# Kernel optimization log

Hardware: AMD Instinct MI355X
Metric: run time of the kernel (lower is better)

## Reference

```python
import jax, jax.numpy as jnp
import numpy as np

B, N, F, H, MH = 8, 1024, 768, 12, 3072
DH = F // H
EPS = 1e-5

def _ln(x, g, b):
    mu = jnp.mean(x, axis=-1, keepdims=True)
    var = jnp.mean(jnp.square(x - mu), axis=-1, keepdims=True)
    return (x - mu) * jax.lax.rsqrt(var + EPS) * g + b

def setup_inputs() -> dict:
    key = jax.random.key(0)
    ks = jax.random.split(key, 16)
    s = 1.0 / np.sqrt(F)
    sm = 1.0 / np.sqrt(MH)
    return {
        "x": jax.random.normal(ks[0], (B, N, F), dtype=jnp.float32),
        "Wq": jax.random.uniform(ks[1], (F, F), jnp.float32, -s, s),
        "bq": jax.random.uniform(ks[2], (F,), jnp.float32, -s, s),
        "Wk": jax.random.uniform(ks[3], (F, F), jnp.float32, -s, s),
        "bk": jax.random.uniform(ks[4], (F,), jnp.float32, -s, s),
        "Wv": jax.random.uniform(ks[5], (F, F), jnp.float32, -s, s),
        "bv": jax.random.uniform(ks[6], (F,), jnp.float32, -s, s),
        "Wo": jax.random.uniform(ks[7], (F, F), jnp.float32, -s, s),
        "bo": jax.random.uniform(ks[8], (F,), jnp.float32, -s, s),
        "ln1_g": jnp.ones((F,), jnp.float32),
        "ln1_b": jnp.zeros((F,), jnp.float32),
        "ln2_g": jnp.ones((F,), jnp.float32),
        "ln2_b": jnp.zeros((F,), jnp.float32),
        "W1": jax.random.uniform(ks[9], (F, MH), jnp.float32, -s, s),
        "b1": jax.random.uniform(ks[10], (MH,), jnp.float32, -s, s),
        "W2": jax.random.uniform(ks[11], (MH, F), jnp.float32, -sm, sm),
        "b2": jax.random.uniform(ks[12], (F,), jnp.float32, -sm, sm),
    }

def reference(x, Wq, bq, Wk, bk, Wv, bv, Wo, bo, ln1_g, ln1_b, ln2_g, ln2_b, W1, b1, W2, b2):
    xn = _ln(x, ln1_g, ln1_b)
    # low-rank (here full-rank, rank=-1) QKV projections, split into heads -> [b,h,n,dh]
    q = (xn @ Wq + bq).reshape(B, N, H, DH).transpose(0, 2, 1, 3)
    k = (xn @ Wk + bk).reshape(B, N, H, DH).transpose(0, 2, 1, 3)
    v = (xn @ Wv + bv).reshape(B, N, H, DH).transpose(0, 2, 1, 3)
    # note: original scales by sqrt(feats), NOT sqrt(d_head)
    score = jax.nn.softmax(jnp.einsum('bhif,bhjf->bhij', q, k) / jnp.sqrt(jnp.float32(F)), axis=-1)
    attn = jnp.einsum('bhij,bhjf->bhif', score, v)
    attn = attn.transpose(0, 2, 1, 3).reshape(B, N, F)
    out = (attn @ Wo + bo) + x  # dropout p=0.0
    h = _ln(out, ln2_g, ln2_b)
    h = jax.nn.gelu(h @ W1 + b1, approximate=False)
    h = jax.nn.gelu(h @ W2 + b2, approximate=False)  # second GELU per source
    return h + out
```

## Files before the change

### kernel.cpp

```cpp
#include <hip/hip_runtime.h>
#include <math.h>

#define B_ 8
#define N_ 1024
#define F_ 768
#define H_ 12
#define DH_ 64
#define MH_ 3072
#define MROWS (B_ * N_)

typedef unsigned short u16;
typedef unsigned int u32;
typedef __bf16 bf16x8 __attribute__((ext_vector_type(8)));
typedef float f32x4 __attribute__((ext_vector_type(4)));

__device__ inline f32x4 mfma16(bf16x8 a, bf16x8 b, f32x4 c) {
  return __builtin_amdgcn_mfma_f32_16x16x32_bf16(a, b, c, 0, 0, 0);
}

__device__ inline u16 f2bu(float f) {
  u32 b = __builtin_bit_cast(u32, f);
  b += 0x7fffu + ((b >> 16) & 1u);
  return (u16)(b >> 16);
}
__device__ inline float bu2f(u16 u) {
  u32 x = ((u32)u) << 16;
  return __builtin_bit_cast(float, x);
}
__device__ inline float gelu_exact(float x) {
  return 0.5f * x * (1.0f + erff(x * 0.70710678118654752f));
}

#define AS1 __attribute__((address_space(1)))
#define AS3 __attribute__((address_space(3)))
__device__ inline void glds16(const void* g, void* l) {
  __builtin_amdgcn_global_load_lds((const AS1 void*)g, (AS3 void*)l, 16, 0, 0);
}

__global__ __launch_bounds__(256) void prep_weights(
    const float* __restrict__ Wq, const float* __restrict__ Wk,
    const float* __restrict__ Wv, const float* __restrict__ Wo,
    const float* __restrict__ W1, const float* __restrict__ W2,
    u16* __restrict__ Wqkvt, u16* __restrict__ Wot,
    u16* __restrict__ W1t, u16* __restrict__ W2t) {
  __shared__ float tile[64][65];
  int z = blockIdx.z;
  const float* in; u16* out; int R, C;
  if (z == 0)      { in = Wq; out = Wqkvt;                       R = 768;  C = 768; }
  else if (z == 1) { in = Wk; out = Wqkvt + 768 * 768;           R = 768;  C = 768; }
  else if (z == 2) { in = Wv; out = Wqkvt + 2 * 768 * 768;       R = 768;  C = 768; }
  else if (z == 3) { in = Wo; out = Wot;                         R = 768;  C = 768; }
  else if (z == 4) { in = W1; out = W1t;                         R = 768;  C = 3072; }
  else             { in = W2; out = W2t;                         R = 3072; C = 768; }
  int r0 = blockIdx.y << 6, c0 = blockIdx.x << 6;
  if (r0 >= R || c0 >= C) return;
  int t = threadIdx.x;
#pragma unroll
  for (int i = 0; i < 16; ++i) {
    int idx = t + (i << 8);
    int r = idx >> 6, c = idx & 63;
    tile[r][c] = in[(size_t)(r0 + r) * C + (c0 + c)];
  }
  __syncthreads();
#pragma unroll
  for (int i = 0; i < 16; ++i) {
    int idx = t + (i << 8);
    int rr = idx >> 6, cc = idx & 63;
    out[(size_t)(c0 + rr) * R + (r0 + cc)] = f2bu(tile[cc][rr]);
  }
}

__global__ __launch_bounds__(256) void transpose_v(
    const u16* __restrict__ in, u16* __restrict__ out, int R, int C) {
  __shared__ float tile[64][65];
  size_t base = (size_t)blockIdx.z * (size_t)R * (size_t)C;
  int r0 = blockIdx.y << 6, c0 = blockIdx.x << 6;
  int t = threadIdx.x;
#pragma unroll
  for (int i = 0; i < 16; ++i) {
    int idx = t + (i << 8);
    int r = idx >> 6, c = idx & 63;
    tile[r][c] = bu2f(in[base + (size_t)(r0 + r) * C + (c0 + c)]);
  }
  __syncthreads();
#pragma unroll
  for (int i = 0; i < 16; ++i) {
    int idx = t + (i << 8);
    int rr = idx >> 6, cc = idx & 63;
    out[base + (size_t)(c0 + rr) * R + (r0 + cc)] = f2bu(tile[cc][rr]);
  }
}

__global__ __launch_bounds__(256) void ln_to_bf16(
    const float* __restrict__ X, const float* __restrict__ gw,
    const float* __restrict__ bw, u16* __restrict__ Y) {
  int row = blockIdx.x;
  int t = threadIdx.x;
  const float* xr = X + (size_t)row * F_;
  float v0 = xr[t], v1 = xr[t + 256], v2 = xr[t + 512];
  float s = v0 + v1 + v2;
  float ss = v0 * v0 + v1 * v1 + v2 * v2;
#pragma unroll
  for (int off = 1; off < 64; off <<= 1) {
    s += __shfl_xor(s, off, 64);
    ss += __shfl_xor(ss, off, 64);
  }
  __shared__ float red[8];
  int wid = t >> 6, lane = t & 63;
  if (lane == 0) { red[wid] = s; red[4 + wid] = ss; }
  __syncthreads();
  s = red[0] + red[1] + red[2] + red[3];
  ss = red[4] + red[5] + red[6] + red[7];
  float mu = s * (1.0f / F_);
  float var = ss * (1.0f / F_) - mu * mu;
  float rstd = rsqrtf(var + 1e-5f);
  u16* yr = Y + (size_t)row * F_;
  yr[t] = f2bu((v0 - mu) * rstd * gw[t] + bw[t]);
  yr[t + 256] = f2bu((v1 - mu) * rstd * gw[t + 256] + bw[t + 256]);
  yr[t + 512] = f2bu((v2 - mu) * rstd * gw[t + 512] + bw[t + 512]);
}

template <int MODE>
__global__ __launch_bounds__(256, 4) void gemm_t(
    const u16* __restrict__ A, const u16* __restrict__ Bt,
    const float* __restrict__ b0, const float* __restrict__ b1,
    const float* __restrict__ b2, void* __restrict__ outp,
    const float* __restrict__ resid, int Ndim, int Kdim, float qscale) {
  __shared__ __attribute__((aligned(16))) u16 As[2][128][32];
  __shared__ __attribute__((aligned(16))) u16 Bs[2][64][32];
  int t = threadIdx.x;
  int lane = t & 63, wid = t >> 6;

  int nwg = gridDim.x;
  int q8 = nwg >> 3;
  int bid = blockIdx.x;
  int swz = (bid & 7) * q8 + (bid >> 3);
  int nnt = Ndim >> 6;
  int mt = swz / nnt, nt = swz - mt * nnt;
  int row0 = mt << 7, col0 = nt << 6;

  int wr = (wid >> 1) << 6;
  int wc = (wid & 1) << 5;
  int lr = lane & 15, lk = (lane >> 4) << 3;
  int rbase = (lane >> 4) << 2;
  f32x4 zero = {0.f, 0.f, 0.f, 0.f};
  f32x4 acc[4][2];
#pragma unroll
  for (int m = 0; m < 4; ++m)
#pragma unroll
    for (int n = 0; n < 2; ++n) acc[m][n] = zero;

  int srow = (wid << 4) + (lane >> 2);
  int scol = (lane & 3) << 3;
  const u16* Ag = A + (size_t)(row0 + srow) * Kdim + scol;
  const u16* Bg = Bt + (size_t)(col0 + srow) * Kdim + scol;
  char* AsB = (char*)&As[0][0][0] + (wid << 10);
  char* BsB = (char*)&Bs[0][0][0] + (wid << 10);
  size_t half = (size_t)64 * Kdim;

  auto STAGE = [&](int buf, int kt) {
    glds16(Ag + kt, AsB + (buf << 13));
    glds16(Ag + kt + half, AsB + (buf << 13) + 4096);
    glds16(Bg + kt, BsB + (buf << 12));
  };

  STAGE(0, 0);
  __syncthreads();
  int nk = Kdim >> 5;
  for (int ki = 0; ki < nk; ++ki) {
    int buf = ki & 1;
    if (ki + 1 < nk) STAGE(buf ^ 1, (ki + 1) << 5);
    bf16x8 af[4], bfr[2];
#pragma unroll
    for (int m = 0; m < 4; ++m) af[m] = *(const bf16x8*)&As[buf][wr + (m << 4) + lr][lk];
#pragma unroll
    for (int n = 0; n < 2; ++n) bfr[n] = *(const bf16x8*)&Bs[buf][wc + (n << 4) + lr][lk];
#pragma unroll
    for (int m = 0; m < 4; ++m)
#pragma unroll
      for (int n = 0; n < 2; ++n) acc[m][n] = mfma16(af[m], bfr[n], acc[m][n]);
    __syncthreads();
  }

#pragma unroll
  for (int n = 0; n < 2; ++n) {
    int col = col0 + wc + (n << 4) + lr;
    float bc;
    int sub = 0, hh = 0, dh = 0;
    float sc = 1.0f;
    if constexpr (MODE == 0) {
      sub = (col >= 1536) ? 2 : (col >= 768 ? 1 : 0);
      int c = col - sub * 768;
      bc = (sub == 0) ? b0[c] : (sub == 1 ? b1[c] : b2[c]);
      hh = c >> 6; dh = c & 63;
      sc = (sub == 0) ? qscale : 1.0f;
    } else {
      bc = b0[col];
    }
#pragma unroll
    for (int m = 0; m < 4; ++m) {
#pragma unroll
      for (int r = 0; r < 4; ++r) {
        int row = row0 + wr + (m << 4) + rbase + r;
        float val = acc[m][n][r] + bc;
        if constexpr (MODE == 0) {
          int bb = row >> 10, nn = row & 1023;
          ((u16*)outp)[(size_t)sub * 6291456 +
                       ((((size_t)bb * H_ + hh) << 10) + nn) * DH_ + dh] = f2bu(val * sc);
        } else if constexpr (MODE == 1) {
          val += resid[(size_t)row * Ndim + col];
          ((float*)outp)[(size_t)row * Ndim + col] = val;
        } else if constexpr (MODE == 2) {
          ((u16*)outp)[(size_t)row * Ndim + col] = f2bu(gelu_exact(val));
        } else {
          val = gelu_exact(val) + resid[(size_t)row * Ndim + col];
          ((float*)outp)[(size_t)row * Ndim + col] = val;
        }
      }
    }
  }
}

__global__ __launch_bounds__(256, 3) void attn_fwd(
    const u16* __restrict__ Q, const u16* __restrict__ K,
    const u16* __restrict__ Vt, u16* __restrict__ Aout) {
  __shared__ __attribute__((aligned(16))) u16 Ks[64][72];
  __shared__ __attribute__((aligned(16))) u16 Vs[64][72];
  __shared__ __attribute__((aligned(16))) u16 Ps[4][32][72];
  int t = threadIdx.x, lane = t & 63, wid = t >> 6;

  int bid = blockIdx.x;
  int swz = (bid & 7) * 96 + (bid >> 3);
  int bh = swz >> 3;
  int qt = swz & 7;
  int q0 = (qt << 7) + (wid << 5);

  int lr = lane & 15, lk = (lane >> 4) << 3;
  int rbase = (lane >> 4) << 2;

  bf16x8 qf[2][2];
#pragma unroll
  for (int m = 0; m < 2; ++m)
#pragma unroll
    for (int ks = 0; ks < 2; ++ks)
      qf[m][ks] = *(const bf16x8*)&Q[((size_t)bh * N_ + q0 + (m << 4) + lr) * DH_ + (ks << 5) + lk];

  float lsum[2][4];
  f32x4 zero = {0.f, 0.f, 0.f, 0.f};
  f32x4 Oacc[2][4];
#pragma unroll
  for (int m = 0; m < 2; ++m) {
#pragma unroll
    for (int r = 0; r < 4; ++r) lsum[m][r] = 0.f;
#pragma unroll
    for (int nd = 0; nd < 4; ++nd) Oacc[m][nd] = zero;
  }

  int srow = t >> 3;
  int scol = (t & 7) << 3;
  const u16* Kg = K + ((size_t)bh * N_ + srow) * DH_ + scol;
  const u16* Vg = Vt + ((size_t)bh * DH_ + srow) * N_ + scol;

  uint4 kr0, kr1, vr0, vr1;
  auto LOADKV = [&](int kt) {
    kr0 = *(const uint4*)(Kg + (size_t)(kt << 6) * DH_);
    kr1 = *(const uint4*)(Kg + (size_t)((kt << 6) + 32) * DH_);
    vr0 = *(const uint4*)(Vg + (kt << 6));
    vr1 = *(const uint4*)(Vg + (size_t)32 * N_ + (kt << 6));
  };
  LOADKV(0);

  for (int kt = 0; kt < 16; ++kt) {
    __syncthreads();
    *(uint4*)&Ks[srow][scol]      = kr0;
    *(uint4*)&Ks[srow + 32][scol] = kr1;
    *(uint4*)&Vs[srow][scol]      = vr0;
    *(uint4*)&Vs[srow + 32][scol] = vr1;
    if (kt + 1 < 16) LOADKV(kt + 1);
    __syncthreads();

    f32x4 s[2][4];
#pragma unroll
    for (int m = 0; m < 2; ++m)
#pragma unroll
      for (int n = 0; n < 4; ++n) s[m][n] = zero;
#pragma unroll
    for (int ks = 0; ks < 2; ++ks) {
      bf16x8 kf[4];
#pragma unroll
      for (int n = 0; n < 4; ++n) kf[n] = *(const bf16x8*)&Ks[(n << 4) + lr][(ks << 5) + lk];
#pragma unroll
      for (int m = 0; m < 2; ++m)
#pragma unroll
        for (int n = 0; n < 4; ++n) s[m][n] = mfma16(qf[m][ks], kf[n], s[m][n]);
    }

#pragma unroll
    for (int m = 0; m < 2; ++m)
#pragma unroll
      for (int n = 0; n < 4; ++n)
#pragma unroll
        for (int r = 0; r < 4; ++r) {
          float p = exp2f(s[m][n][r]);
          lsum[m][r] += p;
          Ps[wid][(m << 4) + rbase + r][(n << 4) + lr] = f2bu(p);
        }

#pragma unroll
    for (int ks = 0; ks < 2; ++ks) {
      bf16x8 pf[2], vf[4];
#pragma unroll
      for (int m = 0; m < 2; ++m) pf[m] = *(const bf16x8*)&Ps[wid][(m << 4) + lr][(ks << 5) + lk];
#pragma unroll
      for (int nd = 0; nd < 4; ++nd) vf[nd] = *(const bf16x8*)&Vs[(nd << 4) + lr][(ks << 5) + lk];
#pragma unroll
      for (int m = 0; m < 2; ++m)
#pragma unroll
        for (int nd = 0; nd < 4; ++nd) Oacc[m][nd] = mfma16(pf[m], vf[nd], Oacc[m][nd]);
    }
  }

  int b = bh / H_, h = bh % H_;
#pragma unroll
  for (int m = 0; m < 2; ++m)
#pragma unroll
    for (int r = 0; r < 4; ++r) {
      float sv = lsum[m][r];
#pragma unroll
      for (int off = 1; off < 16; off <<= 1) sv += __shfl_xor(sv, off, 64);
      float inv = 1.0f / sv;
      int row = q0 + (m << 4) + rbase + r;
      size_t orow = ((size_t)b * N_ + row) * F_ + (size_t)h * DH_;
#pragma unroll
      for (int nd = 0; nd < 4; ++nd)
        Aout[orow + (nd << 4) + lr] = f2bu(Oacc[m][nd][r] * inv);
    }
}

extern "C" void kernel_launch(void* const* d_in, const int* in_sizes, int n_in,
                              void* d_out, int out_size, void* d_ws, size_t ws_size,
                              hipStream_t stream) {
  (void)in_sizes; (void)n_in; (void)out_size; (void)ws_size;
  const float* x   = (const float*)d_in[0];
  const float* Wq  = (const float*)d_in[1];
  const float* bq  = (const float*)d_in[2];
  const float* Wk  = (const float*)d_in[3];
  const float* bk  = (const float*)d_in[4];
  const float* Wv  = (const float*)d_in[5];
  const float* bv  = (const float*)d_in[6];
  const float* Wo  = (const float*)d_in[7];
  const float* bo  = (const float*)d_in[8];
  const float* g1  = (const float*)d_in[9];
  const float* bn1 = (const float*)d_in[10];
  const float* g2  = (const float*)d_in[11];
  const float* bn2 = (const float*)d_in[12];
  const float* W1  = (const float*)d_in[13];
  const float* b1  = (const float*)d_in[14];
  const float* W2  = (const float*)d_in[15];
  const float* b2  = (const float*)d_in[16];

  char* ws = (char*)d_ws;
  size_t off = 0;
  auto alloc = [&](size_t bytes) {
    char* p = ws + off;
    off += (bytes + 255) & ~(size_t)255;
    return p;
  };
  u16* Wqkvt = (u16*)alloc((size_t)3 * F_ * F_ * 2);
  u16* Wot  = (u16*)alloc((size_t)F_ * F_ * 2);
  u16* W1t  = (u16*)alloc((size_t)MH_ * F_ * 2);
  u16* W2t  = (u16*)alloc((size_t)MH_ * F_ * 2);
  u16* xn  = (u16*)alloc((size_t)MROWS * F_ * 2);
  u16* qb  = (u16*)alloc((size_t)B_ * H_ * N_ * DH_ * 2);
  u16* kb  = (u16*)alloc((size_t)B_ * H_ * N_ * DH_ * 2);
  u16* vb  = (u16*)alloc((size_t)B_ * H_ * N_ * DH_ * 2);
  u16* vt  = (u16*)alloc((size_t)B_ * H_ * N_ * DH_ * 2);
  u16* attn = (u16*)alloc((size_t)MROWS * F_ * 2);
  float* outb = (float*)alloc((size_t)MROWS * F_ * 4);
  u16* h1 = qb;
  u16* hn = xn;

  const float QSCALE = 0.052058773227f;

  dim3 blk(256);
  prep_weights<<<dim3(48, 48, 6), blk, 0, stream>>>(Wq, Wk, Wv, Wo, W1, W2,
                                                    Wqkvt, Wot, W1t, W2t);
  ln_to_bf16<<<dim3(MROWS), blk, 0, stream>>>(x, g1, bn1, xn);
  gemm_t<0><<<dim3(64 * 36), blk, 0, stream>>>(xn, Wqkvt, bq, bk, bv, qb,
                                               nullptr, 3 * F_, F_, QSCALE);
  transpose_v<<<dim3(1, 16, 96), blk, 0, stream>>>(vb, vt, N_, DH_);
  attn_fwd<<<dim3(768), blk, 0, stream>>>(qb, kb, vt, attn);
  gemm_t<1><<<dim3(64 * 12), blk, 0, stream>>>(attn, Wot, bo, nullptr, nullptr,
                                               outb, x, F_, F_, 1.0f);
  ln_to_bf16<<<dim3(MROWS), blk, 0, stream>>>(outb, g2, bn2, hn);
  gemm_t<2><<<dim3(64 * 48), blk, 0, stream>>>(hn, W1t, b1, nullptr, nullptr,
                                               h1, nullptr, MH_, F_, 1.0f);
  gemm_t<3><<<dim3(64 * 12), blk, 0, stream>>>(h1, W2t, b2, nullptr, nullptr,
                                               d_out, outb, F_, MH_, 1.0f);
}
```

Before: 317.7 us.

## Write V pre-transposed, store residual in bf16, use tanh-form GELU

The QKV GEMM epilogue now writes V directly in transposed [b,h,dh,n] layout, which removes the separate transpose_v kernel and its extra pass over memory. The attention-output residual buffer is stored as bf16 instead of fp32, halving its traffic into the second LayerNorm and the final GEMM. Exact erf GELU is replaced by a tanh approximation built on exp2, which is cheaper in the epilogues but deviates from the reference's exact GELU. The bf16 residual adds rounding error to the skip path, and the transposed V stores are strided, so their coalescing gets worse.

```diff
diff --git a/kernel.cpp b/kernel.cpp
--- a/kernel.cpp
+++ b/kernel.cpp
@@ -27,8 +27,12 @@
   u32 x = ((u32)u) << 16;
   return __builtin_bit_cast(float, x);
 }
-__device__ inline float gelu_exact(float x) {
-  return 0.5f * x * (1.0f + erff(x * 0.70710678118654752f));
+__device__ inline float gelu_f(float x) {
+  float u = x * (0.7978845608028654f + 0.035677408136300125f * x * x);
+  float t = exp2f(-2.8853900817779268f * fabsf(u));
+  float th = (1.0f - t) / (1.0f + t);
+  th = copysignf(th, u);
+  return 0.5f * x * (1.0f + th);
 }
 
 #define AS1 __attribute__((address_space(1)))
@@ -70,34 +74,17 @@
   }
 }
 
-__global__ __launch_bounds__(256) void transpose_v(
-    const u16* __restrict__ in, u16* __restrict__ out, int R, int C) {
-  __shared__ float tile[64][65];
-  size_t base = (size_t)blockIdx.z * (size_t)R * (size_t)C;
-  int r0 = blockIdx.y << 6, c0 = blockIdx.x << 6;
-  int t = threadIdx.x;
-#pragma unroll
-  for (int i = 0; i < 16; ++i) {
-    int idx = t + (i << 8);
-    int r = idx >> 6, c = idx & 63;
-    tile[r][c] = bu2f(in[base + (size_t)(r0 + r) * C + (c0 + c)]);
-  }
-  __syncthreads();
-#pragma unroll
-  for (int i = 0; i < 16; ++i) {
-    int idx = t + (i << 8);
-    int rr = idx >> 6, cc = idx & 63;
-    out[base + (size_t)(c0 + rr) * R + (r0 + cc)] = f2bu(tile[cc][rr]);
-  }
-}
-
+__device__ inline float ldf(const float* p) { return *p; }
+__device__ inline float ldf(const u16* p) { return bu2f(*p); }
+
+template <typename Tin>
 __global__ __launch_bounds__(256) void ln_to_bf16(
-    const float* __restrict__ X, const float* __restrict__ gw,
+    const Tin* __restrict__ X, const float* __restrict__ gw,
     const float* __restrict__ bw, u16* __restrict__ Y) {
   int row = blockIdx.x;
   int t = threadIdx.x;
-  const float* xr = X + (size_t)row * F_;
-  float v0 = xr[t], v1 = xr[t + 256], v2 = xr[t + 512];
+  const Tin* xr = X + (size_t)row * F_;
+  float v0 = ldf(&xr[t]), v1 = ldf(&xr[t + 256]), v2 = ldf(&xr[t + 512]);
   float s = v0 + v1 + v2;
   float ss = v0 * v0 + v1 * v1 + v2 * v2;
 #pragma unroll
@@ -125,7 +112,7 @@
     const u16* __restrict__ A, const u16* __restrict__ Bt,
     const float* __restrict__ b0, const float* __restrict__ b1,
     const float* __restrict__ b2, void* __restrict__ outp,
-    const float* __restrict__ resid, int Ndim, int Kdim, float qscale) {
+    const void* __restrict__ resid, int Ndim, int Kdim, float qscale) {
   __shared__ __attribute__((aligned(16))) u16 As[2][128][32];
   __shared__ __attribute__((aligned(16))) u16 Bs[2][64][32];
   int t = threadIdx.x;
@@ -205,15 +192,20 @@
         float val = acc[m][n][r] + bc;
         if constexpr (MODE == 0) {
           int bb = row >> 10, nn = row & 1023;
-          ((u16*)outp)[(size_t)sub * 6291456 +
-                       ((((size_t)bb * H_ + hh) << 10) + nn) * DH_ + dh] = f2bu(val * sc);
+          if (sub < 2) {
+            ((u16*)outp)[(size_t)sub * 6291456 +
+                         ((((size_t)bb * H_ + hh) << 10) + nn) * DH_ + dh] = f2bu(val * sc);
+          } else {
+            ((u16*)outp)[(size_t)2 * 6291456 +
+                         ((((size_t)bb * H_ + hh) << 6) + dh) * 1024 + nn] = f2bu(val);
+          }
         } else if constexpr (MODE == 1) {
-          val += resid[(size_t)row * Ndim + col];
-          ((float*)outp)[(size_t)row * Ndim + col] = val;
+          val += ((const float*)resid)[(size_t)row * Ndim + col];
+          ((u16*)outp)[(size_t)row * Ndim + col] = f2bu(val);
         } else if constexpr (MODE == 2) {
-          ((u16*)outp)[(size_t)row * Ndim + col] = f2bu(gelu_exact(val));
+          ((u16*)outp)[(size_t)row * Ndim + col] = f2bu(gelu_f(val));
         } else {
-          val = gelu_exact(val) + resid[(size_t)row * Ndim + col];
+          val = gelu_f(val) + bu2f(((const u16*)resid)[(size_t)row * Ndim + col]);
           ((float*)outp)[(size_t)row * Ndim + col] = val;
         }
       }
@@ -373,26 +365,26 @@
   u16* xn  = (u16*)alloc((size_t)MROWS * F_ * 2);
   u16* qb  = (u16*)alloc((size_t)B_ * H_ * N_ * DH_ * 2);
   u16* kb  = (u16*)alloc((size_t)B_ * H_ * N_ * DH_ * 2);
-  u16* vb  = (u16*)alloc((size_t)B_ * H_ * N_ * DH_ * 2);
   u16* vt  = (u16*)alloc((size_t)B_ * H_ * N_ * DH_ * 2);
+  u16* pad = (u16*)alloc((size_t)B_ * H_ * N_ * DH_ * 2);
   u16* attn = (u16*)alloc((size_t)MROWS * F_ * 2);
-  float* outb = (float*)alloc((size_t)MROWS * F_ * 4);
+  u16* outb = (u16*)alloc((size_t)MROWS * F_ * 2);
   u16* h1 = qb;
   u16* hn = xn;
+  (void)pad;
 
   const float QSCALE = 0.052058773227f;
 
   dim3 blk(256);
   prep_weights<<<dim3(48, 48, 6), blk, 0, stream>>>(Wq, Wk, Wv, Wo, W1, W2,
                                                     Wqkvt, Wot, W1t, W2t);
-  ln_to_bf16<<<dim3(MROWS), blk, 0, stream>>>(x, g1, bn1, xn);
+  ln_to_bf16<float><<<dim3(MROWS), blk, 0, stream>>>(x, g1, bn1, xn);
   gemm_t<0><<<dim3(64 * 36), blk, 0, stream>>>(xn, Wqkvt, bq, bk, bv, qb,
                                                nullptr, 3 * F_, F_, QSCALE);
-  transpose_v<<<dim3(1, 16, 96), blk, 0, stream>>>(vb, vt, N_, DH_);
   attn_fwd<<<dim3(768), blk, 0, stream>>>(qb, kb, vt, attn);
   gemm_t<1><<<dim3(64 * 12), blk, 0, stream>>>(attn, Wot, bo, nullptr, nullptr,
                                                outb, x, F_, F_, 1.0f);
-  ln_to_bf16<<<dim3(MROWS), blk, 0, stream>>>(outb, g2, bn2, hn);
+  ln_to_bf16<u16><<<dim3(MROWS), blk, 0, stream>>>(outb, g2, bn2, hn);
   gemm_t<2><<<dim3(64 * 48), blk, 0, stream>>>(hn, W1t, b1, nullptr, nullptr,
                                                h1, nullptr, MH_, F_, 1.0f);
   gemm_t<3><<<dim3(64 * 12), blk, 0, stream>>>(h1, W2t, b2, nullptr, nullptr,
```

Result: no change. 317.1 us (-0.2%).
